# Kernel tuning notes

Measured on AMD Instinct MI355X. Metric: run time of the kernel, lower is better.

Reference implementation:

```python
import jax, jax.numpy as jnp
import numpy as np

EPS = 1e-5


def _bn_silu(x, gamma, beta):
    # train-mode BatchNorm2d (biased batch stats over N,H,W) followed by SiLU
    m = jnp.mean(x, axis=(0, 2, 3), keepdims=True)
    v = jnp.var(x, axis=(0, 2, 3), keepdims=True)
    y = gamma[None, :, None, None] * (x - m) * jax.lax.rsqrt(v + EPS) + beta[None, :, None, None]
    return y * jax.nn.sigmoid(y)


def _deform_conv2d(x, offset, w, b):
    # x: [B,C,H,W]; offset: [B,2*9,H,W] as (dy,dx) pairs per 3x3 tap; w: [Co,C,3,3]
    B, C, H, W = x.shape
    Co = w.shape[0]
    off = offset.reshape(B, 9, 2, H, W)
    k = jnp.arange(9)
    ky = (k // 3 - 1).astype(x.dtype)  # kernel tap offsets, pad=1 so centered
    kx = (k % 3 - 1).astype(x.dtype)
    py = jnp.arange(H, dtype=x.dtype)[None, None, :, None] + ky[None, :, None, None] + off[:, :, 0]
    px = jnp.arange(W, dtype=x.dtype)[None, None, None, :] + kx[None, :, None, None] + off[:, :, 1]
    y0 = jnp.floor(py)
    x0 = jnp.floor(px)
    wy1 = py - y0
    wx1 = px - x0
    xf = x.reshape(B, C, H * W)

    def corner(yi, xi, cw):
        # zero-padded bilinear corner: mask out-of-bounds taps via weight
        valid = (yi >= 0) & (yi < H) & (xi >= 0) & (xi < W)
        idx = jnp.clip(yi, 0, H - 1) * W + jnp.clip(xi, 0, W - 1)
        g = jnp.take_along_axis(xf, idx.reshape(B, 1, -1), axis=2).reshape(B, C, 9, H, W)
        return g * (cw * valid.astype(x.dtype))[:, None]

    y0i = y0.astype(jnp.int32)
    x0i = x0.astype(jnp.int32)
    s = corner(y0i, x0i, (1 - wy1) * (1 - wx1))
    s = s + corner(y0i, x0i + 1, (1 - wy1) * wx1)
    s = s + corner(y0i + 1, x0i, wy1 * (1 - wx1))
    s = s + corner(y0i + 1, x0i + 1, wy1 * wx1)
    out = jnp.einsum('bckhw,ock->bohw', s, w.reshape(Co, C, 9))
    return out + b[None, :, None, None]


def _conv_transpose(x, w, stride, pad):
    # torch ConvTranspose2d: weight layout [Cin, Cout, kh, kw]
    k = w.shape[2]
    wf = jnp.flip(w, (2, 3)).transpose(1, 0, 2, 3)  # -> OIHW, spatially flipped
    p = k - 1 - pad
    return jax.lax.conv_general_dilated(
        x, wf, (1, 1), [(p, p), (p, p)], lhs_dilation=(stride, stride),
        dimension_numbers=('NCHW', 'OIHW', 'NCHW'))


def setup_inputs() -> dict:
    key = jax.random.key(0)
    ks = jax.random.split(key, 4)
    B, C, Co, H, W = 16, 256, 256, 32, 32
    r = lambda k, s, sc: jax.random.normal(k, s, jnp.float32) * sc
    return {
        'x': r(ks[0], (B, C, H, W), 1.0),
        'w_off': r(ks[1], (18, C, 3, 3), 0.01),
        'b_off': jnp.zeros((18,), jnp.float32),
        'w_def': r(ks[2], (Co, C, 3, 3), 0.02),
        'b_def': jnp.zeros((Co,), jnp.float32),
        'gamma1': jnp.ones((Co,), jnp.float32),
        'beta1': jnp.zeros((Co,), jnp.float32),
        'w_dc': r(ks[3], (Co, Co, 4, 4), 0.02),
        'gamma2': jnp.ones((Co,), jnp.float32),
        'beta2': jnp.zeros((Co,), jnp.float32),
    }


def reference(x, w_off, b_off, w_def, b_def, gamma1, beta1, w_dc, gamma2, beta2):
    offset = jax.lax.conv_general_dilated(
        x, w_off, (1, 1), [(1, 1), (1, 1)],
        dimension_numbers=('NCHW', 'OIHW', 'NCHW')) + b_off[None, :, None, None]
    y = _deform_conv2d(x, offset, w_def, b_def)
    y = _bn_silu(y, gamma1, beta1)
    y = _conv_transpose(y, w_dc, 2, 1)
    return _bn_silu(y, gamma2, beta2)
```

## Files before the change

kernel.cpp:

```cpp
#include <hip/hip_runtime.h>
#include <math.h>

#ifdef __has_builtin
#if __has_builtin(__builtin_amdgcn_global_load_lds)
#define HAS_GLL 1
#endif
#endif
#ifndef HAS_GLL
#define HAS_GLL 0
#endif

typedef __attribute__((ext_vector_type(8))) short short8v;
typedef __attribute__((ext_vector_type(4))) float float4v;

__device__ __forceinline__ unsigned short f2bf(float f) {
    unsigned int u = __float_as_uint(f);
    u += 0x7fffu + ((u >> 16) & 1u);
    return (unsigned short)(u >> 16);
}

__device__ __forceinline__ float silu(float y) { return y / (1.f + expf(-y)); }

__device__ __forceinline__ void stage1k(const void* gsrc, void* ldsbase) {
#if HAS_GLL
    __builtin_amdgcn_global_load_lds((const __attribute__((address_space(1))) unsigned int*)gsrc,
                                     (__attribute__((address_space(3))) unsigned int*)ldsbase,
                                     16, 0, 0);
#else
    int lane = threadIdx.x & 63;
    *(float4*)((char*)ldsbase + lane * 16) = *(const float4*)gsrc;
#endif
}

__global__ __launch_bounds__(256) void k_prep_xt(const float* __restrict__ x,
                                                 unsigned short* __restrict__ xT) {
    int hw0 = blockIdx.x * 32, c0 = blockIdx.y * 32, b = blockIdx.z;
    int t = threadIdx.x;
    __shared__ unsigned short tl[32][36];
    {
        int c_l = t >> 3, w4 = (t & 7) * 4;
        float4 v = *(const float4*)&x[(size_t)((b * 256 + c0 + c_l) * 1024) + hw0 + w4];
        tl[c_l][w4 + 0] = f2bf(v.x);
        tl[c_l][w4 + 1] = f2bf(v.y);
        tl[c_l][w4 + 2] = f2bf(v.z);
        tl[c_l][w4 + 3] = f2bf(v.w);
    }
    __syncthreads();
    {
        int hw_l = t >> 3, c4 = (t & 7) * 4;
        unsigned int s0 = tl[c4 + 0][hw_l];
        unsigned int s1 = tl[c4 + 1][hw_l];
        unsigned int s2 = tl[c4 + 2][hw_l];
        unsigned int s3 = tl[c4 + 3][hw_l];
        uint2 pk;
        pk.x = s0 | (s1 << 16);
        pk.y = s2 | (s3 << 16);
        *(uint2*)&xT[(size_t)((b * 1024 + hw0 + hw_l) * 256) + c0 + c4] = pk;
    }
}

__global__ void k_prep_aoff(const float* __restrict__ w_off, unsigned short* __restrict__ A2off) {
    int i = blockIdx.x * 256 + threadIdx.x;
    int slot = i & 31;
    int oc = (i >> 5) & 31;
    int rest = i >> 10;
    int tap = rest % 9;
    int cc8 = rest / 9;
    int cgrp = (slot >> 3) ^ ((oc >> 1) & 3);
    int c = cc8 * 32 + (cgrp << 3) + (slot & 7);
    unsigned short v = 0;
    if (oc < 18) v = f2bf(w_off[(size_t)oc * 2304 + c * 9 + tap]);
    A2off[i] = v;
}

__global__ void k_prep_a1(const float* __restrict__ w_def, unsigned short* __restrict__ A1) {
    int i = blockIdx.x * 256 + threadIdx.x;
    A1[i] = f2bf(w_def[i]);
}

__global__ void k_prep_a2(const float* __restrict__ w_dc, unsigned short* __restrict__ A2) {
    int i = blockIdx.x * 256 + threadIdx.x;
    int ci = i & 255;
    int tq = (i >> 8) & 3;
    int co = (i >> 10) & 255;
    int p  = i >> 18;
    int ph = p >> 1, pw = p & 1;
    int ty = tq >> 1, tx = tq & 1;
    int kh = 2 * ty + 1 - ph;
    int kw = 2 * tx + 1 - pw;
    A2[i] = f2bf(w_dc[((ci * 256 + co) * 4 + kh) * 4 + kw]);
}

__global__ __launch_bounds__(256) void k_off_gemm(const unsigned short* __restrict__ A2off,
                                                  const unsigned short* __restrict__ xT,
                                                  const float* __restrict__ b_off,
                                                  float* __restrict__ off) {
    int hp = blockIdx.x, b = blockIdx.y;
    int h0 = hp * 2;
    int t = threadIdx.x;
    int lane = t & 63, wid = t >> 6;
    int l15 = lane & 15, g = lane >> 4;
    int swg = (l15 >> 1) & 3;
    __shared__ __align__(16) unsigned short As[9 * 32 * 32];
    __shared__ __align__(16) unsigned short Bsx[4 * 34 * 32];
    float4v acc[2];
    float4v z = {0.f, 0.f, 0.f, 0.f};
    acc[0] = z; acc[1] = z;

    int pos = wid * 16 + l15;
    int py = pos >> 5, px = pos & 31;

    for (int cc8 = 0; cc8 < 8; ++cc8) {
        __syncthreads();
        for (int idx = t; idx < 1152; idx += 256)
            stage1k(A2off + (size_t)cc8 * 9216 + idx * 8, (char*)As + idx * 16);
        for (int idx = t; idx < 544; idx += 256) {
            int r = idx / 136;
            int rem = idx - r * 136;
            int col = rem >> 2;
            int sgrp = rem & 3;
            int grp = sgrp ^ ((col >> 1) & 3);
            int h = h0 - 1 + r;
            int w = col - 1;
            uint4 v = {0u, 0u, 0u, 0u};
            if (h >= 0 && h < 32 && w >= 0 && w < 32)
                v = *(const uint4*)&xT[(size_t)((b * 1024 + h * 32 + w) * 256) + cc8 * 32 + grp * 8];
            *(uint4*)((char*)Bsx + ((r * 34 + col) << 6) + (sgrp << 4)) = v;
        }
        __syncthreads();
#pragma unroll
        for (int tap = 0; tap < 9; ++tap) {
            int ky = tap / 3, kx = tap - ky * 3;
            int col = px + kx;
            int rowr = py + ky;
            short8v bbf = *(const short8v*)((const char*)Bsx + ((rowr * 34 + col) << 6) +
                                            ((g ^ ((col >> 1) & 3)) << 4));
            short8v a0 = *(const short8v*)((const char*)As + tap * 2048 + l15 * 64 + ((g ^ swg) << 4));
            short8v a1 = *(const short8v*)((const char*)As + tap * 2048 + (16 + l15) * 64 + ((g ^ swg) << 4));
            acc[0] = __builtin_amdgcn_mfma_f32_16x16x32_bf16(a0, bbf, acc[0], 0, 0, 0);
            acc[1] = __builtin_amdgcn_mfma_f32_16x16x32_bf16(a1, bbf, acc[1], 0, 0, 0);
        }
    }
    int h = h0 + py;
#pragma unroll
    for (int r = 0; r < 4; ++r) {
        int oc = g * 4 + r;
        off[((size_t)(b * 18 + oc) << 10) + (h << 5) + px] = acc[0][r] + b_off[oc];
    }
    if (g == 0) {
#pragma unroll
        for (int r = 0; r < 2; ++r) {
            int oc = 16 + r;
            off[((size_t)(b * 18 + oc) << 10) + (h << 5) + px] = acc[1][r] + b_off[oc];
        }
    }
}

__global__ __launch_bounds__(576) void k_sample(const float* __restrict__ x,
                                                const float* __restrict__ off,
                                                unsigned short* __restrict__ S) {
    int cg = blockIdx.x, b = blockIdx.y, half = blockIdx.z;
    int cbase = cg * 8;
    int t = threadIdx.x;
    int k = t >> 6, lane = t & 63;
    __shared__ __align__(16) unsigned int xpl[4 * 1156];
    __shared__ __align__(16) unsigned short sS[72 * 66];

    for (int u = t; u < 1024; u += 576) {
        int p = u >> 8, row = (u >> 3) & 31, cq = (u & 7) << 2;
        const float* src0 = x + ((size_t)(b * 256 + cbase + 2 * p) << 10) + (row << 5) + cq;
        float4 a = *(const float4*)src0;
        float4 c = *(const float4*)(src0 + 1024);
        uint4 pk;
        pk.x = (unsigned int)f2bf(a.x) | ((unsigned int)f2bf(c.x) << 16);
        pk.y = (unsigned int)f2bf(a.y) | ((unsigned int)f2bf(c.y) << 16);
        pk.z = (unsigned int)f2bf(a.z) | ((unsigned int)f2bf(c.z) << 16);
        pk.w = (unsigned int)f2bf(a.w) | ((unsigned int)f2bf(c.w) << 16);
        *(uint4*)&xpl[p * 1156 + row * 36 + cq] = pk;
    }

    int wr_row = t / 9, wr_q = t - wr_row * 9;
    const float* offk0 = off + ((size_t)(b * 18 + 2 * k) << 10);
    const float* offk1 = off + ((size_t)(b * 18 + 2 * k + 1) << 10);
    int ky = k / 3 - 1, kx = k % 3 - 1;
    __syncthreads();

    for (int ci = 0; ci < 8; ++ci) {
        int chunk = half * 8 + ci;
        int pos = chunk * 64 + lane;
        int h = pos >> 5, w = pos & 31;
        float dy = offk0[pos];
        float dx = offk1[pos];
        float py = (float)(h + ky) + dy;
        float px = (float)(w + kx) + dx;
        float fy = floorf(py), fx = floorf(px);
        int y0i = (int)fy, x0i = (int)fx;
        float wy = py - fy, wxf = px - fx;
        float vy0 = (y0i >= 0 && y0i < 32) ? 1.f : 0.f;
        float vy1 = (y0i >= -1 && y0i < 31) ? 1.f : 0.f;
        float vx0 = (x0i >= 0 && x0i < 32) ? 1.f : 0.f;
        float vx1 = (x0i >= -1 && x0i < 31) ? 1.f : 0.f;
        int y0c = min(max(y0i, 0), 31), y1c = min(max(y0i + 1, 0), 31);
        int x0c = min(max(x0i, 0), 31), x1c = min(max(x0i + 1, 0), 31);
        float w00 = (1.f - wy) * (1.f - wxf) * vy0 * vx0;
        float w01 = (1.f - wy) * wxf * vy0 * vx1;
        float w10 = wy * (1.f - wxf) * vy1 * vx0;
        float w11 = wy * wxf * vy1 * vx1;
        int a00 = y0c * 36 + x0c, a01 = y0c * 36 + x1c;
        int a10 = y1c * 36 + x0c, a11 = y1c * 36 + x1c;
#pragma unroll
        for (int p = 0; p < 4; ++p) {
            const unsigned int* pl = xpl + p * 1156;
            unsigned int c00 = pl[a00], c01 = pl[a01], c10 = pl[a10], c11 = pl[a11];
            float e00 = __uint_as_float(c00 << 16), o00 = __uint_as_float(c00 & 0xFFFF0000u);
            float e01 = __uint_as_float(c01 << 16), o01 = __uint_as_float(c01 & 0xFFFF0000u);
            float e10 = __uint_as_float(c10 << 16), o10 = __uint_as_float(c10 & 0xFFFF0000u);
            float e11 = __uint_as_float(c11 << 16), o11 = __uint_as_float(c11 & 0xFFFF0000u);
            float ve = w00 * e00 + w01 * e01 + w10 * e10 + w11 * e11;
            float vo = w00 * o00 + w01 * o01 + w10 * o10 + w11 * o11;
            sS[((2 * p) * 9 + k) * 66 + lane] = f2bf(ve);
            sS[((2 * p + 1) * 9 + k) * 66 + lane] = f2bf(vo);
        }
        __syncthreads();
        {
            int basekc = wr_q * 8;
            unsigned int s0 = sS[(basekc + 0) * 66 + wr_row];
            unsigned int s1 = sS[(basekc + 1) * 66 + wr_row];
            unsigned int s2 = sS[(basekc + 2) * 66 + wr_row];
            unsigned int s3 = sS[(basekc + 3) * 66 + wr_row];
            unsigned int s4 = sS[(basekc + 4) * 66 + wr_row];
            unsigned int s5 = sS[(basekc + 5) * 66 + wr_row];
            unsigned int s6 = sS[(basekc + 6) * 66 + wr_row];
            unsigned int s7 = sS[(basekc + 7) * 66 + wr_row];
            uint4 qv;
            qv.x = s0 | (s1 << 16);
            qv.y = s2 | (s3 << 16);
            qv.z = s4 | (s5 << 16);
            qv.w = s6 | (s7 << 16);
            *(uint4*)(S + (size_t)(b * 1024 + chunk * 64 + wr_row) * 2304 + cg * 72 + wr_q * 8) = qv;
        }
        __syncthreads();
    }
}

__global__ __launch_bounds__(256) void k_gemm1(const unsigned short* __restrict__ A1,
                                               const unsigned short* __restrict__ S,
                                               const float* __restrict__ b_def,
                                               float* __restrict__ y1) {
    int nb = blockIdx.x, mb = blockIdx.y;
    int t = threadIdx.x;
    int lane = t & 63, wid = t >> 6;
    int wm = wid >> 1, wn = wid & 1;
    __shared__ __align__(16) unsigned short As[128 * 32];
    __shared__ __align__(16) unsigned short Bs[64 * 32];
    int m0 = mb * 128, n0 = nb * 64;
    float4v acc[4][2];
    float4v z = {0.f, 0.f, 0.f, 0.f};
#pragma unroll
    for (int i = 0; i < 4; ++i) { acc[i][0] = z; acc[i][1] = z; }
    int rQ = lane >> 2;
    int qA = (lane & 3) ^ ((lane >> 3) & 3);
    const unsigned short* gA0 = A1 + (size_t)(m0 + wid * 32 + rQ) * 2304 + qA * 8;
    const unsigned short* gA1 = gA0 + (size_t)16 * 2304;
    const unsigned short* gB0 = S + (size_t)(n0 + wid * 16 + rQ) * 2304 + qA * 8;
    unsigned short* lA0 = As + wid * 32 * 32;
    unsigned short* lA1 = As + (wid * 32 + 16) * 32;
    unsigned short* lB0 = Bs + wid * 16 * 32;
    int g = lane >> 4, l15 = lane & 15;
    int gs = (g ^ ((l15 >> 1) & 3)) << 4;
    for (int s = 0; s < 72; ++s) {
        __syncthreads();
        stage1k(gA0 + s * 32, lA0);
        stage1k(gA1 + s * 32, lA1);
        stage1k(gB0 + s * 32, lB0);
        __syncthreads();
        short8v a[4], bb[2];
#pragma unroll
        for (int mi = 0; mi < 4; ++mi)
            a[mi] = *(const short8v*)((const char*)As + ((wm * 64 + mi * 16 + l15) * 64 + gs));
#pragma unroll
        for (int ni = 0; ni < 2; ++ni)
            bb[ni] = *(const short8v*)((const char*)Bs + ((wn * 32 + ni * 16 + l15) * 64 + gs));
#pragma unroll
        for (int mi = 0; mi < 4; ++mi)
#pragma unroll
            for (int ni = 0; ni < 2; ++ni)
                acc[mi][ni] = __builtin_amdgcn_mfma_f32_16x16x32_bf16(a[mi], bb[ni], acc[mi][ni], 0, 0, 0);
    }
    int b = n0 >> 10;
    int posb = n0 & 1023;
#pragma unroll
    for (int mi = 0; mi < 4; ++mi) {
#pragma unroll
        for (int r = 0; r < 4; ++r) {
            int co = m0 + wm * 64 + mi * 16 + g * 4 + r;
            float bv = b_def[co];
            float* dst = y1 + ((size_t)(b * 256 + co) << 10) + posb;
#pragma unroll
            for (int ni = 0; ni < 2; ++ni)
                dst[wn * 32 + ni * 16 + l15] = acc[mi][ni][r] + bv;
        }
    }
}

__global__ __launch_bounds__(256) void k_gemm2(const unsigned short* __restrict__ A2,
                                               const unsigned short* __restrict__ y1T,
                                               float* __restrict__ outP,
                                               float* __restrict__ pstats2) {
    int nb = blockIdx.x, mb = blockIdx.y, p = blockIdx.z;
    int ph = p >> 1, pw = p & 1;
    int t = threadIdx.x;
    int lane = t & 63, wid = t >> 6;
    int wm = wid >> 1, wn = wid & 1;
    int l15 = lane & 15, g = lane >> 4;
    __shared__ __align__(16) unsigned short As[128 * 64];
    __shared__ __align__(16) unsigned short Bs[128 * 64];
    int m0 = mb * 128, n0 = nb * 128;
    int b = n0 >> 10, pos0 = n0 & 1023, oh0 = pos0 >> 5;

    int dtab[4];
#pragma unroll
    for (int tap = 0; tap < 4; ++tap) {
        int ty = tap >> 1, tx = tap & 1;
        int dy = ph ? (1 - ty) : (-ty);
        int dx = pw ? (1 - tx) : (-tx);
        dtab[tap] = (dy * 34 + dx) * 256;
    }
    const unsigned short* srcA[4];
    const unsigned short* srcB[4];
    unsigned short* dstA[4];
    unsigned short* dstB[4];
#pragma unroll
    for (int it = 0; it < 4; ++it) {
        int idx = t + it * 256;
        int r = idx >> 3, s8 = idx & 7, c = s8 ^ (r & 7);
        srcA[it] = A2 + (size_t)(p * 256 + m0 + r) * 1024 + c * 8;
        dstA[it] = As + idx * 8;
        int ih = oh0 + (r >> 5) + 1;
        int iw = (r & 31) + 1;
        srcB[it] = y1T + ((size_t)(b * 34 + ih) * 34 + iw) * 256 + c * 8;
        dstB[it] = Bs + idx * 8;
    }

    float4v acc[4][4];
    float4v z = {0.f, 0.f, 0.f, 0.f};
#pragma unroll
    for (int i = 0; i < 4; ++i)
#pragma unroll
        for (int j = 0; j < 4; ++j) acc[i][j] = z;

    for (int step = 0; step < 16; ++step) {
        int tap = step >> 2;
        int koff = step * 64;
        int boff = dtab[tap] + (step & 3) * 64;
        __syncthreads();
#pragma unroll
        for (int it = 0; it < 4; ++it) {
            stage1k(srcA[it] + koff, dstA[it]);
            stage1k(srcB[it] + boff, dstB[it]);
        }
        __syncthreads();
#pragma unroll
        for (int kk = 0; kk < 2; ++kk) {
            short8v a[4], bb[4];
#pragma unroll
            for (int mi = 0; mi < 4; ++mi) {
                int row = wm * 64 + mi * 16 + l15;
                int slot = ((kk << 2) + g) ^ (row & 7);
                a[mi] = *(const short8v*)((const char*)As + row * 128 + slot * 16);
            }
#pragma unroll
            for (int ni = 0; ni < 4; ++ni) {
                int row = wn * 64 + ni * 16 + l15;
                int slot = ((kk << 2) + g) ^ (row & 7);
                bb[ni] = *(const short8v*)((const char*)Bs + row * 128 + slot * 16);
            }
#pragma unroll
            for (int mi = 0; mi < 4; ++mi)
#pragma unroll
                for (int ni = 0; ni < 4; ++ni)
                    acc[mi][ni] = __builtin_amdgcn_mfma_f32_16x16x32_bf16(a[mi], bb[ni], acc[mi][ni], 0, 0, 0);
        }
    }
#pragma unroll
    for (int mi = 0; mi < 4; ++mi) {
#pragma unroll
        for (int r = 0; r < 4; ++r) {
            int co = m0 + wm * 64 + mi * 16 + g * 4 + r;
            float* dst = outP + ((size_t)((p * 16 + b) * 256 + co) << 10) + pos0;
#pragma unroll
            for (int ni = 0; ni < 4; ++ni)
                dst[wn * 64 + ni * 16 + l15] = acc[mi][ni][r];
        }
    }
    __syncthreads();
    float* sred  = (float*)As;
    float* s2red = sred + 256;
#pragma unroll
    for (int mi = 0; mi < 4; ++mi) {
#pragma unroll
        for (int r = 0; r < 4; ++r) {
            float s = 0.f, s2 = 0.f;
#pragma unroll
            for (int ni = 0; ni < 4; ++ni) {
                float v = acc[mi][ni][r];
                s += v;
                s2 += v * v;
            }
#pragma unroll
            for (int m = 8; m >= 1; m >>= 1) {
                s  += __shfl_xor(s, m, 64);
                s2 += __shfl_xor(s2, m, 64);
            }
            if (l15 == 0) {
                int col = wm * 64 + mi * 16 + g * 4 + r;
                sred[col * 2 + wn]  = s;
                s2red[col * 2 + wn] = s2;
            }
        }
    }
    __syncthreads();
    if (t < 128) {
        float s  = sred[t * 2] + sred[t * 2 + 1];
        float s2 = s2red[t * 2] + s2red[t * 2 + 1];
        int row = p * 128 + nb;
        int ch = mb * 128 + t;
        pstats2[ch * 512 + row] = s;
        pstats2[131072 + ch * 512 + row] = s2;
    }
}

__global__ __launch_bounds__(256) void k_bnstats_part(const float* __restrict__ src, int nparts,
                                                      float* __restrict__ pstats) {
    int ch = blockIdx.x, j = blockIdx.y;
    int t = threadIdx.x;
    const float* p = src + ((size_t)(j * 256 + ch) << 10);
    float4 v = *(const float4*)&p[t * 4];
    float s  = v.x + v.y + v.z + v.w;
    float s2 = v.x * v.x + v.y * v.y + v.z * v.z + v.w * v.w;
    __shared__ float rs[256], rs2[256];
    rs[t] = s; rs2[t] = s2;
    __syncthreads();
    for (int d = 128; d > 0; d >>= 1) {
        if (t < d) { rs[t] += rs[t + d]; rs2[t] += rs2[t + d]; }
        __syncthreads();
    }
    if (t == 0) {
        pstats[ch * nparts + j] = rs[0];
        pstats[256 * nparts + ch * nparts + j] = rs2[0];
    }
}

__global__ __launch_bounds__(256) void k_bnfin(const float* __restrict__ pstats, int nparts, float n,
                                               float* __restrict__ mean, float* __restrict__ rstd) {
    int ch = threadIdx.x;
    float s = 0.f, s2 = 0.f;
    for (int j = 0; j < nparts; ++j) {
        s += pstats[ch * nparts + j];
        s2 += pstats[256 * nparts + ch * nparts + j];
    }
    float m = s / n;
    float var = s2 / n - m * m;
    mean[ch] = m;
    rstd[ch] = rsqrtf(var + 1e-5f);
}

__global__ __launch_bounds__(256) void k_bnfin2(const float* __restrict__ pstats2,
                                                float* __restrict__ mean, float* __restrict__ rstd) {
    int ch = blockIdx.x;
    int t = threadIdx.x;
    float s  = pstats2[ch * 512 + t] + pstats2[ch * 512 + 256 + t];
    float s2 = pstats2[131072 + ch * 512 + t] + pstats2[131072 + ch * 512 + 256 + t];
    __shared__ float rs[256], rs2[256];
    rs[t] = s; rs2[t] = s2;
    __syncthreads();
    for (int d = 128; d > 0; d >>= 1) {
        if (t < d) { rs[t] += rs[t + d]; rs2[t] += rs2[t + d]; }
        __syncthreads();
    }
    if (t == 0) {
        float n = 65536.f;
        float m = rs[0] / n;
        float var = rs2[0] / n - m * m;
        mean[ch] = m;
        rstd[ch] = rsqrtf(var + 1e-5f);
    }
}

__global__ __launch_bounds__(256) void k_bnsilu_padT(const float* __restrict__ y1,
                                                     const float* __restrict__ mean,
                                                     const float* __restrict__ rstd,
                                                     const float* __restrict__ gamma,
                                                     const float* __restrict__ beta,
                                                     unsigned short* __restrict__ y1T) {
    int py = blockIdx.x, cg = blockIdx.y, b = blockIdx.z;
    int c0 = cg * 32;
    int t = threadIdx.x;
    __shared__ unsigned short tl[32][36];
    {
        int c_l = t >> 3, px4 = (t & 7) * 4;
        int ch = c0 + c_l;
        float m = mean[ch], rs = rstd[ch], ga = gamma[ch], be = beta[ch];
        float4 v = *(const float4*)&y1[(size_t)((b * 256 + ch) << 10) + (py << 5) + px4];
        tl[c_l][px4 + 0] = f2bf(silu(ga * (v.x - m) * rs + be));
        tl[c_l][px4 + 1] = f2bf(silu(ga * (v.y - m) * rs + be));
        tl[c_l][px4 + 2] = f2bf(silu(ga * (v.z - m) * rs + be));
        tl[c_l][px4 + 3] = f2bf(silu(ga * (v.w - m) * rs + be));
    }
    __syncthreads();
    {
        int px = t >> 3, c4 = (t & 7) * 4;
        unsigned int s0 = tl[c4 + 0][px];
        unsigned int s1 = tl[c4 + 1][px];
        unsigned int s2 = tl[c4 + 2][px];
        unsigned int s3 = tl[c4 + 3][px];
        uint2 pk;
        pk.x = s0 | (s1 << 16);
        pk.y = s2 | (s3 << 16);
        *(uint2*)&y1T[((size_t)(b * 34 + py + 1) * 34 + (px + 1)) * 256 + c0 + c4] = pk;
    }
}

__global__ __launch_bounds__(256) void k_bnsilu_out(const float* __restrict__ outP,
                                                    const float* __restrict__ mean,
                                                    const float* __restrict__ rstd,
                                                    const float* __restrict__ gamma,
                                                    const float* __restrict__ beta,
                                                    float* __restrict__ out) {
    unsigned int i = blockIdx.x * 256 + threadIdx.x;
    int ow4 = i & 15;
    int oh = (i >> 4) & 63;
    int co = (i >> 10) & 255;
    int b  = i >> 18;
    int p0 = (oh & 1) * 2;
    int pos = ((oh >> 1) << 5) + ow4 * 2;
    const float* pl0 = outP + ((size_t)((p0 * 16 + b) * 256 + co) << 10) + pos;
    const float* pl1 = pl0 + ((size_t)16 * 256 << 10);
    float2 e = *(const float2*)pl0;
    float2 o = *(const float2*)pl1;
    float m = mean[co], rs = rstd[co], ga = gamma[co], be = beta[co];
    float4 v;
    v.x = silu(ga * (e.x - m) * rs + be);
    v.y = silu(ga * (o.x - m) * rs + be);
    v.z = silu(ga * (e.y - m) * rs + be);
    v.w = silu(ga * (o.y - m) * rs + be);
    *(float4*)&out[((size_t)(b * 256 + co) << 12) + (oh << 6) + ow4 * 4] = v;
}

extern "C" void kernel_launch(void* const* d_in, const int* in_sizes, int n_in,
                              void* d_out, int out_size, void* d_ws, size_t ws_size,
                              hipStream_t stream) {
    const float* x      = (const float*)d_in[0];
    const float* w_off  = (const float*)d_in[1];
    const float* b_off  = (const float*)d_in[2];
    const float* w_def  = (const float*)d_in[3];
    const float* b_def  = (const float*)d_in[4];
    const float* gamma1 = (const float*)d_in[5];
    const float* beta1  = (const float*)d_in[6];
    const float* w_dc   = (const float*)d_in[7];
    const float* gamma2 = (const float*)d_in[8];
    const float* beta2  = (const float*)d_in[9];
    float* out = (float*)d_out;

    char* base = (char*)d_ws;
    unsigned short* S    = (unsigned short*)base;
    float*          y1   = (float*)(base + 75497472);
    unsigned short* y1T  = (unsigned short*)(base + 92274688);
    unsigned short* A1   = (unsigned short*)(base + 101744640);
    unsigned short* A2   = (unsigned short*)(base + 102924288);
    float*          off  = (float*)(base + 105021440);
    float*          stats = (float*)(base + 106201088);
    float* mean1 = stats, *rstd1 = stats + 256, *mean2 = stats + 512, *rstd2 = stats + 768;
    float* pstats = off;
    float* pstats2 = off;
    unsigned short* xT    = (unsigned short*)base;
    unsigned short* A2off = (unsigned short*)(base + 8388608);
    float* outP = (float*)base;

    k_prep_a1<<<2304, 256, 0, stream>>>(w_def, A1);
    k_prep_a2<<<4096, 256, 0, stream>>>(w_dc, A2);
    k_prep_aoff<<<288, 256, 0, stream>>>(w_off, A2off);
    k_prep_xt<<<dim3(32, 8, 16), 256, 0, stream>>>(x, xT);
    k_off_gemm<<<dim3(16, 16), 256, 0, stream>>>(A2off, xT, b_off, off);
    k_sample<<<dim3(32, 16, 2), 576, 0, stream>>>(x, off, S);
    k_gemm1<<<dim3(256, 2), 256, 0, stream>>>(A1, S, b_def, y1);
    k_bnstats_part<<<dim3(256, 16), 256, 0, stream>>>(y1, 16, pstats);
    k_bnfin<<<1, 256, 0, stream>>>(pstats, 16, 16384.f, mean1, rstd1);
    hipMemsetAsync(y1T, 0, 9469952, stream);
    k_bnsilu_padT<<<dim3(32, 8, 16), 256, 0, stream>>>(y1, mean1, rstd1, gamma1, beta1, y1T);
    k_gemm2<<<dim3(128, 2, 4), 256, 0, stream>>>(A2, y1T, outP, pstats2);
    k_bnfin2<<<256, 256, 0, stream>>>(pstats2, mean2, rstd2);
    k_bnsilu_out<<<16384, 256, 0, stream>>>(outP, mean2, rstd2, gamma2, beta2, out);
}
```

Measured before the change: 212.4 us.

## Fuse BN1 stats into gemm1, double-buffer gemm2, store gemm2 output as bf16

The first BatchNorm's partial sums are now computed in the gemm1 epilogue, which removes the separate stats kernel and its re-read of y1. k_bnfin then reduces 256 partials per channel instead of 16. gemm2 double-buffers its LDS tiles, so the next K-step's global-to-LDS staging overlaps the current MFMA work, at the cost of twice the LDS. gemm2 also writes its intermediate output as bf16 rather than fp32, halving that write and the final kernel's read, with some precision loss in the pre-BN values.

```diff
diff --git a/kernel.cpp b/kernel.cpp
--- a/kernel.cpp
+++ b/kernel.cpp
@@ -246,7 +246,8 @@
 __global__ __launch_bounds__(256) void k_gemm1(const unsigned short* __restrict__ A1,
                                                const unsigned short* __restrict__ S,
                                                const float* __restrict__ b_def,
-                                               float* __restrict__ y1) {
+                                               float* __restrict__ y1,
+                                               float* __restrict__ pstats1) {
     int nb = blockIdx.x, mb = blockIdx.y;
     int t = threadIdx.x;
     int lane = t & 63, wid = t >> 6;
@@ -287,8 +288,11 @@
             for (int ni = 0; ni < 2; ++ni)
                 acc[mi][ni] = __builtin_amdgcn_mfma_f32_16x16x32_bf16(a[mi], bb[ni], acc[mi][ni], 0, 0, 0);
     }
+    __syncthreads();
     int b = n0 >> 10;
     int posb = n0 & 1023;
+    float* sred  = (float*)As;
+    float* s2red = sred + 256;
 #pragma unroll
     for (int mi = 0; mi < 4; ++mi) {
 #pragma unroll
@@ -296,16 +300,39 @@
             int co = m0 + wm * 64 + mi * 16 + g * 4 + r;
             float bv = b_def[co];
             float* dst = y1 + ((size_t)(b * 256 + co) << 10) + posb;
-#pragma unroll
-            for (int ni = 0; ni < 2; ++ni)
-                dst[wn * 32 + ni * 16 + l15] = acc[mi][ni][r] + bv;
-        }
+            float s = 0.f, s2 = 0.f;
+#pragma unroll
+            for (int ni = 0; ni < 2; ++ni) {
+                float v = acc[mi][ni][r] + bv;
+                dst[wn * 32 + ni * 16 + l15] = v;
+                s += v;
+                s2 += v * v;
+            }
+#pragma unroll
+            for (int m = 8; m >= 1; m >>= 1) {
+                s  += __shfl_xor(s, m, 64);
+                s2 += __shfl_xor(s2, m, 64);
+            }
+            if (l15 == 0) {
+                int col = wm * 64 + mi * 16 + g * 4 + r;
+                sred[col * 2 + wn]  = s;
+                s2red[col * 2 + wn] = s2;
+            }
+        }
+    }
+    __syncthreads();
+    if (t < 128) {
+        float s  = sred[t * 2] + sred[t * 2 + 1];
+        float s2 = s2red[t * 2] + s2red[t * 2 + 1];
+        int ch = m0 + t;
+        pstats1[ch * 256 + nb] = s;
+        pstats1[65536 + ch * 256 + nb] = s2;
     }
 }
 
 __global__ __launch_bounds__(256) void k_gemm2(const unsigned short* __restrict__ A2,
                                                const unsigned short* __restrict__ y1T,
-                                               float* __restrict__ outP,
+                                               unsigned short* __restrict__ outP,
                                                float* __restrict__ pstats2) {
     int nb = blockIdx.x, mb = blockIdx.y, p = blockIdx.z;
     int ph = p >> 1, pw = p & 1;
@@ -313,8 +340,8 @@
     int lane = t & 63, wid = t >> 6;
     int wm = wid >> 1, wn = wid & 1;
     int l15 = lane & 15, g = lane >> 4;
-    __shared__ __align__(16) unsigned short As[128 * 64];
-    __shared__ __align__(16) unsigned short Bs[128 * 64];
+    __shared__ __align__(16) unsigned short As[2][8192];
+    __shared__ __align__(16) unsigned short Bs[2][8192];
     int m0 = mb * 128, n0 = nb * 128;
     int b = n0 >> 10, pos0 = n0 & 1023, oh0 = pos0 >> 5;
 
@@ -328,18 +355,16 @@
     }
     const unsigned short* srcA[4];
     const unsigned short* srcB[4];
-    unsigned short* dstA[4];
-    unsigned short* dstB[4];
+    int dstoff[4];
 #pragma unroll
     for (int it = 0; it < 4; ++it) {
         int idx = t + it * 256;
         int r = idx >> 3, s8 = idx & 7, c = s8 ^ (r & 7);
         srcA[it] = A2 + (size_t)(p * 256 + m0 + r) * 1024 + c * 8;
-        dstA[it] = As + idx * 8;
         int ih = oh0 + (r >> 5) + 1;
         int iw = (r & 31) + 1;
         srcB[it] = y1T + ((size_t)(b * 34 + ih) * 34 + iw) * 256 + c * 8;
-        dstB[it] = Bs + idx * 8;
+        dstoff[it] = idx * 8;
     }
 
     float4v acc[4][4];
@@ -349,17 +374,26 @@
 #pragma unroll
         for (int j = 0; j < 4; ++j) acc[i][j] = z;
 
+#pragma unroll
+    for (int it = 0; it < 4; ++it) {
+        stage1k(srcA[it], &As[0][dstoff[it]]);
+        stage1k(srcB[it] + dtab[0], &Bs[0][dstoff[it]]);
+    }
+    __syncthreads();
+
     for (int step = 0; step < 16; ++step) {
-        int tap = step >> 2;
-        int koff = step * 64;
-        int boff = dtab[tap] + (step & 3) * 64;
-        __syncthreads();
-#pragma unroll
-        for (int it = 0; it < 4; ++it) {
-            stage1k(srcA[it] + koff, dstA[it]);
-            stage1k(srcB[it] + boff, dstB[it]);
-        }
-        __syncthreads();
+        int cur = step & 1;
+        if (step < 15) {
+            int ns = step + 1;
+            int tap = ns >> 2;
+            int koff = ns * 64;
+            int boff = dtab[tap] + (ns & 3) * 64;
+#pragma unroll
+            for (int it = 0; it < 4; ++it) {
+                stage1k(srcA[it] + koff, &As[cur ^ 1][dstoff[it]]);
+                stage1k(srcB[it] + boff, &Bs[cur ^ 1][dstoff[it]]);
+            }
+        }
 #pragma unroll
         for (int kk = 0; kk < 2; ++kk) {
             short8v a[4], bb[4];
@@ -367,13 +401,13 @@
             for (int mi = 0; mi < 4; ++mi) {
                 int row = wm * 64 + mi * 16 + l15;
                 int slot = ((kk << 2) + g) ^ (row & 7);
-                a[mi] = *(const short8v*)((const char*)As + row * 128 + slot * 16);
+                a[mi] = *(const short8v*)((const char*)&As[cur][0] + row * 128 + slot * 16);
             }
 #pragma unroll
             for (int ni = 0; ni < 4; ++ni) {
                 int row = wn * 64 + ni * 16 + l15;
                 int slot = ((kk << 2) + g) ^ (row & 7);
-                bb[ni] = *(const short8v*)((const char*)Bs + row * 128 + slot * 16);
+                bb[ni] = *(const short8v*)((const char*)&Bs[cur][0] + row * 128 + slot * 16);
             }
 #pragma unroll
             for (int mi = 0; mi < 4; ++mi)
@@ -381,20 +415,20 @@
                 for (int ni = 0; ni < 4; ++ni)
                     acc[mi][ni] = __builtin_amdgcn_mfma_f32_16x16x32_bf16(a[mi], bb[ni], acc[mi][ni], 0, 0, 0);
         }
+        __syncthreads();
     }
 #pragma unroll
     for (int mi = 0; mi < 4; ++mi) {
 #pragma unroll
         for (int r = 0; r < 4; ++r) {
             int co = m0 + wm * 64 + mi * 16 + g * 4 + r;
-            float* dst = outP + ((size_t)((p * 16 + b) * 256 + co) << 10) + pos0;
+            unsigned short* dst = outP + ((size_t)((p * 16 + b) * 256 + co) << 10) + pos0;
 #pragma unroll
             for (int ni = 0; ni < 4; ++ni)
-                dst[wn * 64 + ni * 16 + l15] = acc[mi][ni][r];
-        }
-    }
-    __syncthreads();
-    float* sred  = (float*)As;
+                dst[wn * 64 + ni * 16 + l15] = f2bf(acc[mi][ni][r]);
+        }
+    }
+    float* sred  = (float*)&As[0][0];
     float* s2red = sred + 256;
 #pragma unroll
     for (int mi = 0; mi < 4; ++mi) {
@@ -424,30 +458,9 @@
         float s  = sred[t * 2] + sred[t * 2 + 1];
         float s2 = s2red[t * 2] + s2red[t * 2 + 1];
         int row = p * 128 + nb;
-        int ch = mb * 128 + t;
+        int ch = m0 + t;
         pstats2[ch * 512 + row] = s;
         pstats2[131072 + ch * 512 + row] = s2;
-    }
-}
-
-__global__ __launch_bounds__(256) void k_bnstats_part(const float* __restrict__ src, int nparts,
-                                                      float* __restrict__ pstats) {
-    int ch = blockIdx.x, j = blockIdx.y;
-    int t = threadIdx.x;
-    const float* p = src + ((size_t)(j * 256 + ch) << 10);
-    float4 v = *(const float4*)&p[t * 4];
-    float s  = v.x + v.y + v.z + v.w;
-    float s2 = v.x * v.x + v.y * v.y + v.z * v.z + v.w * v.w;
-    __shared__ float rs[256], rs2[256];
-    rs[t] = s; rs2[t] = s2;
-    __syncthreads();
-    for (int d = 128; d > 0; d >>= 1) {
-        if (t < d) { rs[t] += rs[t + d]; rs2[t] += rs2[t + d]; }
-        __syncthreads();
-    }
-    if (t == 0) {
-        pstats[ch * nparts + j] = rs[0];
-        pstats[256 * nparts + ch * nparts + j] = rs2[0];
     }
 }
 
@@ -521,7 +534,7 @@
     }
 }
 
-__global__ __launch_bounds__(256) void k_bnsilu_out(const float* __restrict__ outP,
+__global__ __launch_bounds__(256) void k_bnsilu_out(const unsigned short* __restrict__ outP,
                                                     const float* __restrict__ mean,
                                                     const float* __restrict__ rstd,
                                                     const float* __restrict__ gamma,
@@ -534,16 +547,18 @@
     int b  = i >> 18;
     int p0 = (oh & 1) * 2;
     int pos = ((oh >> 1) << 5) + ow4 * 2;
-    const float* pl0 = outP + ((size_t)((p0 * 16 + b) * 256 + co) << 10) + pos;
-    const float* pl1 = pl0 + ((size_t)16 * 256 << 10);
-    float2 e = *(const float2*)pl0;
-    float2 o = *(const float2*)pl1;
+    const unsigned short* pl0 = outP + ((size_t)((p0 * 16 + b) * 256 + co) << 10) + pos;
+    const unsigned short* pl1 = pl0 + ((size_t)16 * 256 << 10);
+    unsigned int ue = *(const unsigned int*)pl0;
+    unsigned int uo = *(const unsigned int*)pl1;
+    float ex = __uint_as_float(ue << 16), ey = __uint_as_float(ue & 0xFFFF0000u);
+    float ox = __uint_as_float(uo << 16), oy = __uint_as_float(uo & 0xFFFF0000u);
     float m = mean[co], rs = rstd[co], ga = gamma[co], be = beta[co];
     float4 v;
-    v.x = silu(ga * (e.x - m) * rs + be);
-    v.y = silu(ga * (o.x - m) * rs + be);
-    v.z = silu(ga * (e.y - m) * rs + be);
-    v.w = silu(ga * (o.y - m) * rs + be);
+    v.x = silu(ga * (ex - m) * rs + be);
+    v.y = silu(ga * (ox - m) * rs + be);
+    v.z = silu(ga * (ey - m) * rs + be);
+    v.w = silu(ga * (oy - m) * rs + be);
     *(float4*)&out[((size_t)(b * 256 + co) << 12) + (oh << 6) + ow4 * 4] = v;
 }
 
@@ -571,11 +586,11 @@
     float*          off  = (float*)(base + 105021440);
     float*          stats = (float*)(base + 106201088);
     float* mean1 = stats, *rstd1 = stats + 256, *mean2 = stats + 512, *rstd2 = stats + 768;
-    float* pstats = off;
+    float* pstats1 = off;
     float* pstats2 = off;
     unsigned short* xT    = (unsigned short*)base;
     unsigned short* A2off = (unsigned short*)(base + 8388608);
-    float* outP = (float*)base;
+    unsigned short* outP = (unsigned short*)base;
 
     k_prep_a1<<<2304, 256, 0, stream>>>(w_def, A1);
     k_prep_a2<<<4096, 256, 0, stream>>>(w_dc, A2);
@@ -583,9 +598,8 @@
     k_prep_xt<<<dim3(32, 8, 16), 256, 0, stream>>>(x, xT);
     k_off_gemm<<<dim3(16, 16), 256, 0, stream>>>(A2off, xT, b_off, off);
     k_sample<<<dim3(32, 16, 2), 576, 0, stream>>>(x, off, S);
-    k_gemm1<<<dim3(256, 2), 256, 0, stream>>>(A1, S, b_def, y1);
-    k_bnstats_part<<<dim3(256, 16), 256, 0, stream>>>(y1, 16, pstats);
-    k_bnfin<<<1, 256, 0, stream>>>(pstats, 16, 16384.f, mean1, rstd1);
+    k_gemm1<<<dim3(256, 2), 256, 0, stream>>>(A1, S, b_def, y1, pstats1);
+    k_bnfin<<<1, 256, 0, stream>>>(pstats1, 256, 16384.f, mean1, rstd1);
     hipMemsetAsync(y1T, 0, 9469952, stream);
     k_bnsilu_padT<<<dim3(32, 8, 16), 256, 0, stream>>>(y1, mean1, rstd1, gamma1, beta1, y1T);
     k_gemm2<<<dim3(128, 2, 4), 256, 0, stream>>>(A2, y1T, outP, pstats2);
```

Result: slower. 262.2 us (+23.5%).
